# Optimization experiments

Hardware: AMD Instinct MI355X
Metric: run time of the kernel (lower is better)

## Reference

```python
import jax, jax.numpy as jnp
import numpy as np

N = 6144      # num_sample / nodes per graph
E = 196608    # edges per graph (avg degree 32)
F = 256       # input feature dim (same for all 4 graphs)
H = 256       # hidden_channels (== F so all SAGEConv layers are HxH)
D = 512       # fusion dim (hardcoded in module)
G = 4         # number of graphs
ATT = 128     # attention bottleneck (hardcoded)
WS = 0.05     # weight init scale


def setup_inputs() -> dict:
    key = jax.random.key(0)
    k = jax.random.split(key, 16)
    return {
        "xs": jax.random.normal(k[0], (G, N, F), jnp.float32),
        "edge_index": jax.random.randint(k[1], (G, 2, E), 0, N),
        "x_content": jax.random.normal(k[2], (N, F), jnp.float32),
        # SAGEConv params: per graph, 3 layers, lin_l (with bias) on aggregated
        # neighbors, lin_r (no bias) on root. F == H so all layers stack.
        "sage_Wl": jax.random.normal(k[3], (G, 3, H, H), jnp.float32) * WS,
        "sage_bl": jnp.zeros((G, 3, H), jnp.float32),
        "sage_Wr": jax.random.normal(k[4], (G, 3, H, H), jnp.float32) * WS,
        # lin1..lin4 : F -> 512
        "lin_W": jax.random.normal(k[5], (G, D, F), jnp.float32) * WS,
        "lin_b": jnp.zeros((G, D), jnp.float32),
        # ResidualFusion attention MLP 512 -> 128 -> 1, softmax over graph axis
        "att_W1": jax.random.normal(k[6], (ATT, D), jnp.float32) * WS,
        "att_b1": jnp.zeros((ATT,), jnp.float32),
        "att_W2": jax.random.normal(k[7], (1, ATT), jnp.float32) * WS,
        "att_b2": jnp.zeros((1,), jnp.float32),
        "res_W": jax.random.normal(k[8], (D, D), jnp.float32) * WS,
        "res_b": jnp.zeros((D,), jnp.float32),
        "fusion_weight": jnp.array([0.7, 0.3], jnp.float32),
        # SelfExpression coefficients, init 1e-8 * ones as in the module
        "C_content": jnp.full((N, N), 1e-8, jnp.float32),
        "C_structure": jnp.full((N, N), 1e-8, jnp.float32),
    }


def _gnn(x, ei, Wl, bl, Wr):
    # One GraphSAGE stack: 3 SAGEConv(mean) layers, relu after each,
    # dropout is identity in eval mode.
    src, dst = ei[0], ei[1]
    deg = jax.ops.segment_sum(jnp.ones((E,), x.dtype), dst, num_segments=N)
    deg = jnp.maximum(deg, 1.0)[:, None]
    for i in range(3):
        m = jax.ops.segment_sum(x[src], dst, num_segments=N) / deg  # mean aggr
        x = jax.nn.relu(m @ Wl[i].T + bl[i] + x @ Wr[i].T)
    return x


def reference(xs, edge_index, x_content, sage_Wl, sage_bl, sage_Wr,
              lin_W, lin_b, att_W1, att_b1, att_W2, att_b2,
              res_W, res_b, fusion_weight, C_content, C_structure):
    # Four GraphSAGE stacks, vmapped over the graph axis.
    xg = jax.vmap(_gnn)(xs, edge_index, sage_Wl, sage_bl, sage_Wr)  # [G,N,F]
    # lin1..lin4 -> [G,N,D]
    feats = jnp.einsum('gnf,gdf->gnd', xg, lin_W) + lin_b[:, None, :]
    # ResidualFusion: attention over stacked features, softmax over graph axis
    h = jax.nn.relu(jnp.einsum('gnd,kd->gnk', feats, att_W1) + att_b1)
    logits = jnp.einsum('gnk,ok->gno', h, att_W2) + att_b2  # [G,N,1]
    w = jax.nn.softmax(logits, axis=0)
    weighted = jnp.sum(w * feats, axis=0)            # [N,D]
    residual = feats[0] @ res_W.T + res_b            # [N,D]
    structure_features = jax.nn.relu(weighted + residual)
    # Coefficient fusion with softmax-normalized scalar weights
    fw = jax.nn.softmax(fusion_weight)
    fusion_expression = fw[0] * C_content + fw[1] * C_structure  # [N,N]
    return (fusion_expression, x_content, structure_features, C_content, C_structure)
```

## Files before the change

### kernel.cpp

```cpp
#include <hip/hip_runtime.h>
#include <hip/hip_bf16.h>

constexpr int N_ = 6144;
constexpr int E_ = 196608;
constexpr int F_ = 256;
constexpr int D_ = 512;
constexpr int G_ = 4;
constexpr int A_ = 128;

typedef short bf16x8 __attribute__((ext_vector_type(8)));
typedef float f32x4 __attribute__((ext_vector_type(4)));
typedef float f4 __attribute__((ext_vector_type(4)));
typedef int i4 __attribute__((ext_vector_type(4)));
typedef __hip_bfloat16 hb;

__device__ inline float b2f(unsigned short u) {
    union { unsigned u32; float f; } x; x.u32 = ((unsigned)u) << 16; return x.f;
}
__device__ inline unsigned short f2bu(float f) {
    hb b = __float2bfloat16(f);
    return *reinterpret_cast<unsigned short*>(&b);
}

#define GLD_LDS16(gp, lp) \
    __builtin_amdgcn_global_load_lds((const __attribute__((address_space(1))) void*)(gp), \
                                     (__attribute__((address_space(3))) void*)(lp), 16, 0, 0)

struct SP {
    const f4* Cc; const f4* Cs; const float* fw;
    f4* o0; f4* o3; f4* o4;
    long ib; long ie; int nsb;
};

__device__ void stream_slice(const SP sp, int sb)
{
    float fa = sp.fw[0], fb = sp.fw[1];
    float mx = fmaxf(fa, fb);
    float ea = expf(fa - mx), eb = expf(fb - mx);
    float w0 = ea / (ea + eb), w1 = eb / (ea + eb);
    const long S = (long)sp.nsb * blockDim.x;
    long i = sp.ib + (long)sb * blockDim.x + threadIdx.x;
    for (; i + 3 * S < sp.ie; i += 4 * S) {
        f4 a0 = __builtin_nontemporal_load(sp.Cc + i);
        f4 b0 = __builtin_nontemporal_load(sp.Cs + i);
        f4 a1 = __builtin_nontemporal_load(sp.Cc + i + S);
        f4 b1 = __builtin_nontemporal_load(sp.Cs + i + S);
        f4 a2 = __builtin_nontemporal_load(sp.Cc + i + 2 * S);
        f4 b2 = __builtin_nontemporal_load(sp.Cs + i + 2 * S);
        f4 a3 = __builtin_nontemporal_load(sp.Cc + i + 3 * S);
        f4 b3 = __builtin_nontemporal_load(sp.Cs + i + 3 * S);
        __builtin_nontemporal_store(a0, sp.o3 + i);
        __builtin_nontemporal_store(b0, sp.o4 + i);
        __builtin_nontemporal_store(w0 * a0 + w1 * b0, sp.o0 + i);
        __builtin_nontemporal_store(a1, sp.o3 + i + S);
        __builtin_nontemporal_store(b1, sp.o4 + i + S);
        __builtin_nontemporal_store(w0 * a1 + w1 * b1, sp.o0 + i + S);
        __builtin_nontemporal_store(a2, sp.o3 + i + 2 * S);
        __builtin_nontemporal_store(b2, sp.o4 + i + 2 * S);
        __builtin_nontemporal_store(w0 * a2 + w1 * b2, sp.o0 + i + 2 * S);
        __builtin_nontemporal_store(a3, sp.o3 + i + 3 * S);
        __builtin_nontemporal_store(b3, sp.o4 + i + 3 * S);
        __builtin_nontemporal_store(w0 * a3 + w1 * b3, sp.o0 + i + 3 * S);
    }
    for (; i < sp.ie; i += S) {
        f4 a = __builtin_nontemporal_load(sp.Cc + i);
        f4 b = __builtin_nontemporal_load(sp.Cs + i);
        __builtin_nontemporal_store(a, sp.o3 + i);
        __builtin_nontemporal_store(b, sp.o4 + i);
        __builtin_nontemporal_store(w0 * a + w1 * b, sp.o0 + i);
    }
}

__global__ void k_tail(SP sp) { stream_slice(sp, blockIdx.x); }

__global__ void k_prep(const float* __restrict__ xc, f4* __restrict__ o1,
                       const float* __restrict__ xs, ushort4* __restrict__ xsb,
                       const float* __restrict__ Wl, ushort4* __restrict__ Wlb,
                       const float* __restrict__ Wr, ushort4* __restrict__ Wrb,
                       const float* __restrict__ lin, ushort4* __restrict__ linb,
                       const float* __restrict__ aw, ushort4* __restrict__ awb,
                       const float* __restrict__ rw, ushort4* __restrict__ rwb,
                       i4* __restrict__ cursz, int PB, SP sp)
{
    if ((int)blockIdx.x < sp.nsb) { stream_slice(sp, blockIdx.x); return; }
    const int cb = blockIdx.x - sp.nsb;
    const long nz = (long)G_ * N_ / 4;
    const long n0 = (long)N_ * F_ / 4;
    const long n1 = (long)G_ * N_ * F_ / 4;
    const long n2 = (long)G_ * 3 * F_ * F_ / 4;
    const long n4 = (long)G_ * D_ * F_ / 4;
    const long n5 = (long)A_ * D_ / 4;
    const long n6 = (long)D_ * D_ / 4;
    const long T = nz + n0 + n1 + 2 * n2 + n4 + n5 + n6;
    long stride = (long)PB * blockDim.x;
    for (long u = (long)cb * blockDim.x + threadIdx.x; u < T; u += stride) {
        long v = u;
        if (v < nz) { cursz[v] = i4{0, 0, 0, 0}; continue; }
        v -= nz;
        if (v < n0) {
            f4 x = __builtin_nontemporal_load((const f4*)xc + v);
            __builtin_nontemporal_store(x, o1 + v);
            continue;
        }
        v -= n0;
        const float* s; ushort4* d;
        if (v < n1) { s = xs; d = xsb; }
        else {
            v -= n1;
            if (v < n2) { s = Wl; d = Wlb; }
            else {
                v -= n2;
                if (v < n2) { s = Wr; d = Wrb; }
                else {
                    v -= n2;
                    if (v < n4) { s = lin; d = linb; }
                    else {
                        v -= n4;
                        if (v < n5) { s = aw; d = awb; }
                        else { v -= n5; s = rw; d = rwb; }
                    }
                }
            }
        }
        f4 x = *((const f4*)s + v);
        ushort4 o;
        o.x = f2bu(x[0]); o.y = f2bu(x[1]); o.z = f2bu(x[2]); o.w = f2bu(x[3]);
        d[v] = o;
    }
}

__global__ void k_count(const int* __restrict__ ei, int* __restrict__ cnt, SP sp)
{
    if ((int)blockIdx.x < sp.nsb) { stream_slice(sp, blockIdx.x); return; }
    long i = (long)(blockIdx.x - sp.nsb) * blockDim.x + threadIdx.x;
    int g = (int)(i / E_);
    int e = (int)(i % E_);
    int dst = ei[(long)g * 2 * E_ + E_ + e];
    atomicAdd(&cnt[g * N_ + dst], 1);
}

__global__ void k_scan(int* __restrict__ cnt_cursor, int* __restrict__ row_ptr,
                       float* __restrict__ deg, SP sp)
{
    if ((int)blockIdx.x < sp.nsb) { stream_slice(sp, blockIdx.x); return; }
    int g = blockIdx.x - sp.nsb;
    __shared__ int sdata[1024];
    __shared__ int s_off;
    if (threadIdx.x == 0) s_off = 0;
    __syncthreads();
    for (int base = 0; base < N_; base += 1024) {
        int idx = g * N_ + base + threadIdx.x;
        int v = cnt_cursor[idx];
        sdata[threadIdx.x] = v;
        __syncthreads();
        for (int d = 1; d < 1024; d <<= 1) {
            int t = (threadIdx.x >= d) ? sdata[threadIdx.x - d] : 0;
            __syncthreads();
            sdata[threadIdx.x] += t;
            __syncthreads();
        }
        int incl = sdata[threadIdx.x];
        int excl = incl - v;
        int rp = s_off + excl;
        row_ptr[g * (N_ + 1) + base + threadIdx.x] = rp;
        cnt_cursor[idx] = rp;
        deg[idx] = (float)(v > 1 ? v : 1);
        __syncthreads();
        if (threadIdx.x == 1023) s_off += incl;
        __syncthreads();
    }
    if (threadIdx.x == 0) row_ptr[g * (N_ + 1) + N_] = s_off;
}

__global__ void k_fill(const int* __restrict__ ei, int* __restrict__ cursor,
                       int* __restrict__ csr_src, SP sp)
{
    if ((int)blockIdx.x < sp.nsb) { stream_slice(sp, blockIdx.x); return; }
    long i = (long)(blockIdx.x - sp.nsb) * blockDim.x + threadIdx.x;
    int g = (int)(i / E_);
    int e = (int)(i % E_);
    int src = ei[(long)g * 2 * E_ + e];
    int dst = ei[(long)g * 2 * E_ + E_ + e];
    int pos = atomicAdd(&cursor[g * N_ + dst], 1);
    csr_src[(long)g * E_ + pos] = src;
}

__global__ __launch_bounds__(256) void k_aggregate(
    const hb* __restrict__ x, const int* __restrict__ csr_src,
    const int* __restrict__ row_ptr, const float* __restrict__ deg,
    hb* __restrict__ m, SP sp)
{
    if ((int)blockIdx.x < sp.nsb) { stream_slice(sp, blockIdx.x); return; }
    int b = blockIdx.x - sp.nsb;
    int g = (b & 7) >> 1;
    int idx = ((b >> 3) << 1) | (b & 1);
    int node = idx * 4 + (threadIdx.x >> 6);
    int lane = threadIdx.x & 63;
    int qq = lane >> 4;
    int l16 = (lane & 15) * 16;
    const hb* xg = x + (long)g * N_ * F_;
    const int* rp = row_ptr + g * (N_ + 1);
    const int* cs = csr_src + (long)g * E_;
    int s = __builtin_amdgcn_readfirstlane(rp[node]);
    int e = __builtin_amdgcn_readfirstlane(rp[node + 1]);
    float a[16] = {};
    #pragma unroll 2
    for (int j = s; j < e; j += 4) {
        if (j + qq < e) {
            int src = cs[j + qq];
            const bf16x8* p = (const bf16x8*)(xg + (long)src * F_ + l16);
            bf16x8 v0 = p[0], v1 = p[1];
            #pragma unroll
            for (int q = 0; q < 8; ++q) a[q]     += b2f((unsigned short)v0[q]);
            #pragma unroll
            for (int q = 0; q < 8; ++q) a[q + 8] += b2f((unsigned short)v1[q]);
        }
    }
    #pragma unroll
    for (int q = 0; q < 16; ++q) {
        a[q] += __shfl_xor(a[q], 16);
        a[q] += __shfl_xor(a[q], 32);
    }
    if (qq == 0) {
        float inv = 1.0f / deg[g * N_ + node];
        bf16x8 lo, hi;
        #pragma unroll
        for (int q = 0; q < 8; ++q) { lo[q] = (short)f2bu(a[q] * inv); hi[q] = (short)f2bu(a[q + 8] * inv); }
        *(bf16x8*)(m + ((long)g * N_ + node) * F_ + l16) = lo;
        *(bf16x8*)(m + ((long)g * N_ + node) * F_ + l16 + 8) = hi;
    }
}

template <bool DUAL, bool RELU, bool LOGITS, bool FUSEOUT, bool PIN>
__global__ __launch_bounds__(256) void k_mfma_nt(
    const hb* __restrict__ A1, const hb* __restrict__ B1,
    const hb* __restrict__ A2, const hb* __restrict__ B2,
    const float* __restrict__ bias, hb* __restrict__ C,
    int ncols, int nrows, int ng, int Nc, int K,
    long a_batch, long b_batch, long bias_batch, long c_batch,
    const float* __restrict__ W2, const float* __restrict__ b2,
    float* __restrict__ logits,
    const float* __restrict__ lgAll, const hb* __restrict__ fAll,
    float* __restrict__ o2,
    SP sp)
{
    if ((int)blockIdx.x < sp.nsb) { stream_slice(sp, blockIdx.x); return; }
    int b = blockIdx.x - sp.nsb;
    int g, col, row;
    if (PIN) {
        g = (b & 7) >> 1;
        int idx = ((b >> 3) << 1) | (b & 1);
        col = idx % ncols; row = idx / ncols;
    } else {
        col = b % ncols;
        int r2 = b / ncols;
        row = r2 % nrows; g = r2 / nrows;
    }
    const int row0 = row * 128;
    const int col0 = col * 128;

    const hb* A1p = A1 + (long)g * a_batch;
    const hb* B1p = B1 + (long)g * b_batch;
    const hb* A2p = nullptr;
    const hb* B2p = nullptr;
    if (DUAL) { A2p = A2 + (long)g * a_batch; B2p = B2 + (long)g * b_batch; }
    const float* biasp = bias + (long)g * bias_batch;
    hb* Cp = C + (long)g * c_batch;

    __shared__ hb As[128 * 64];
    __shared__ hb Bs[128 * 64];
    __shared__ float sLog[2][128];
    __shared__ float sW[128][4];

    const int tid = threadIdx.x;
    const int lane = tid & 63;
    const int wid = tid >> 6;
    const int wr = wid >> 1;
    const int wc = wid & 1;

    if (FUSEOUT) {
        if (tid < 128) {
            int rr = row0 + tid;
            float l0 = lgAll[rr], l1 = lgAll[N_ + rr], l2 = lgAll[2 * N_ + rr], l3 = lgAll[3 * N_ + rr];
            float mx = fmaxf(fmaxf(l0, l1), fmaxf(l2, l3));
            float e0 = expf(l0 - mx), e1 = expf(l1 - mx), e2 = expf(l2 - mx), e3 = expf(l3 - mx);
            float inv = 1.f / (e0 + e1 + e2 + e3);
            sW[tid][0] = e0 * inv; sW[tid][1] = e1 * inv;
            sW[tid][2] = e2 * inv; sW[tid][3] = e3 * inv;
        }
    }

    const int srow = tid >> 3;
    const int sk8  = (tid & 7) * 8;

    f32x4 acc[4][4] = {};

    const int fr  = lane & 15;
    const int fkq = (lane >> 4) * 8;

    const int npass = DUAL ? 2 : 1;
    for (int pass = 0; pass < npass; ++pass) {
        const hb* A = (DUAL && pass) ? A2p : A1p;
        const hb* B = (DUAL && pass) ? B2p : B1p;
        for (int k0 = 0; k0 < K; k0 += 64) {
            __syncthreads();
            #pragma unroll
            for (int c = 0; c < 4; ++c) {
                int r = c * 32 + srow;
                GLD_LDS16(A + (long)(row0 + r) * K + k0 + sk8, As + r * 64 + sk8);
                GLD_LDS16(B + (long)(col0 + r) * K + k0 + sk8, Bs + r * 64 + sk8);
            }
            __syncthreads();

            bf16x8 af[4][2], bfr[4][2];
            #pragma unroll
            for (int m = 0; m < 4; ++m)
                #pragma unroll
                for (int kk = 0; kk < 2; ++kk)
                    af[m][kk] = *(const bf16x8*)(As + (wr * 64 + m * 16 + fr) * 64 + kk * 32 + fkq);
            #pragma unroll
            for (int n = 0; n < 4; ++n)
                #pragma unroll
                for (int kk = 0; kk < 2; ++kk)
                    bfr[n][kk] = *(const bf16x8*)(Bs + (wc * 64 + n * 16 + fr) * 64 + kk * 32 + fkq);

            #pragma unroll
            for (int m = 0; m < 4; ++m)
                #pragma unroll
                for (int n = 0; n < 4; ++n)
                    #pragma unroll
                    for (int kk = 0; kk < 2; ++kk)
                        acc[m][n] = __builtin_amdgcn_mfma_f32_16x16x32_bf16(
                            af[m][kk], bfr[n][kk], acc[m][n], 0, 0, 0);
        }
    }

    const int r4 = (lane >> 4) * 4;
    const int cc = lane & 15;

    if (LOGITS) {
        float w2v[4], bv[4];
        #pragma unroll
        for (int n = 0; n < 4; ++n) {
            int c2 = wc * 64 + n * 16 + cc;
            w2v[n] = W2[c2];
            bv[n]  = biasp[c2];
        }
        #pragma unroll
        for (int m = 0; m < 4; ++m) {
            #pragma unroll
            for (int j = 0; j < 4; ++j) {
                float p = 0.f;
                #pragma unroll
                for (int n = 0; n < 4; ++n) {
                    float h = fmaxf(acc[m][n][j] + bv[n], 0.f);
                    p += h * w2v[n];
                }
                p += __shfl_xor(p, 1); p += __shfl_xor(p, 2);
                p += __shfl_xor(p, 4); p += __shfl_xor(p, 8);
                if (cc == 0) sLog[wc][wr * 64 + m * 16 + r4 + j] = p;
            }
        }
        __syncthreads();
        if (tid < 128)
            logits[(long)g * N_ + row0 + tid] = sLog[0][tid] + sLog[1][tid] + b2[0];
    } else if (FUSEOUT) {
        const unsigned short* fu = (const unsigned short*)fAll;
        #pragma unroll
        for (int m = 0; m < 4; ++m) {
            #pragma unroll
            for (int n = 0; n < 4; ++n) {
                int c2 = col0 + wc * 64 + n * 16 + cc;
                float bv = biasp[c2];
                #pragma unroll
                for (int j = 0; j < 4; ++j) {
                    int rl = wr * 64 + m * 16 + r4 + j;
                    int rr = row0 + rl;
                    float s = acc[m][n][j] + bv;
                    #pragma unroll
                    for (int gg = 0; gg < 4; ++gg)
                        s += sW[rl][gg] * b2f(fu[((long)gg * N_ + rr) * D_ + c2]);
                    __builtin_nontemporal_store(fmaxf(s, 0.f), o2 + (long)rr * D_ + c2);
                }
            }
        }
    } else {
        #pragma unroll
        for (int m = 0; m < 4; ++m) {
            #pragma unroll
            for (int n = 0; n < 4; ++n) {
                int c2 = col0 + wc * 64 + n * 16 + cc;
                float bv = biasp[c2];
                #pragma unroll
                for (int j = 0; j < 4; ++j) {
                    int rr = row0 + wr * 64 + m * 16 + r4 + j;
                    float v = acc[m][n][j] + bv;
                    if (RELU) v = fmaxf(v, 0.f);
                    Cp[(long)rr * Nc + c2] = __float2bfloat16(v);
                }
            }
        }
    }
}

extern "C" void kernel_launch(void* const* d_in, const int* in_sizes, int n_in,
                              void* d_out, int out_size, void* d_ws, size_t ws_size,
                              hipStream_t stream)
{
    const float* xs        = (const float*)d_in[0];
    const int*   ei        = (const int*)  d_in[1];
    const float* x_content = (const float*)d_in[2];
    const float* sage_Wl   = (const float*)d_in[3];
    const float* sage_bl   = (const float*)d_in[4];
    const float* sage_Wr   = (const float*)d_in[5];
    const float* lin_W     = (const float*)d_in[6];
    const float* lin_b     = (const float*)d_in[7];
    const float* att_W1    = (const float*)d_in[8];
    const float* att_b1    = (const float*)d_in[9];
    const float* att_W2    = (const float*)d_in[10];
    const float* att_b2    = (const float*)d_in[11];
    const float* res_W     = (const float*)d_in[12];
    const float* res_b     = (const float*)d_in[13];
    const float* fusion_w  = (const float*)d_in[14];
    const float* Cc        = (const float*)d_in[15];
    const float* Cs        = (const float*)d_in[16];

    float* out0 = (float*)d_out;
    float* out1 = out0 + (size_t)N_ * N_;
    float* out2 = out1 + (size_t)N_ * F_;
    float* out3 = out2 + (size_t)N_ * D_;
    float* out4 = out3 + (size_t)N_ * N_;

    char* w = (char*)d_ws;
    auto alloc = [&](size_t bytes) {
        char* p = w;
        w += (bytes + 255) & ~(size_t)255;
        return p;
    };
    hb* xsb   = (hb*)alloc((size_t)G_ * N_ * F_ * 2);
    hb* xA    = (hb*)alloc((size_t)G_ * N_ * F_ * 2);
    hb* xB    = (hb*)alloc((size_t)G_ * N_ * F_ * 2);
    hb* mb    = (hb*)alloc((size_t)G_ * N_ * F_ * 2);
    hb* feats = (hb*)alloc((size_t)G_ * N_ * D_ * 2);
    hb* Wlb   = (hb*)alloc((size_t)G_ * 3 * F_ * F_ * 2);
    hb* Wrb   = (hb*)alloc((size_t)G_ * 3 * F_ * F_ * 2);
    hb* linWb = (hb*)alloc((size_t)G_ * D_ * F_ * 2);
    hb* attWb = (hb*)alloc((size_t)A_ * D_ * 2);
    hb* resWb = (hb*)alloc((size_t)D_ * D_ * 2);
    float* logit = (float*)alloc((size_t)G_ * N_ * 4);
    float* deg   = (float*)alloc((size_t)G_ * N_ * 4);
    int*   rowp  = (int*)  alloc((size_t)G_ * (N_ + 1) * 4);
    int*   curs  = (int*)  alloc((size_t)G_ * N_ * 4);
    int*   csrc  = (int*)  alloc((size_t)G_ * E_ * 4);

    const long U = (long)N_ * N_ / 4;
    const int cum[14] = {0, 85, 115, 135, 175, 285, 360, 470, 545, 655, 730, 820, 870, 975};
    long B[14];
    for (int i = 0; i < 14; ++i) B[i] = U * cum[i] / 1000;
    const int PREPB   = 512;
    const int SB_PREP = 512;
    const int SB_FLAT = 256;
    const int SB_GEMM = 256;
    const int TAILB   = 1024;
    auto mkSP = [&](int i, int nsb) {
        SP sp;
        sp.Cc = (const f4*)Cc; sp.Cs = (const f4*)Cs; sp.fw = fusion_w;
        sp.o0 = (f4*)out0; sp.o3 = (f4*)out3; sp.o4 = (f4*)out4;
        sp.ib = B[i]; sp.ie = (i == 13) ? U : B[i + 1]; sp.nsb = nsb;
        return sp;
    };
    SP tail = mkSP(13, TAILB);

    k_prep<<<SB_PREP + PREPB, 256, 0, stream>>>(
        x_content, (f4*)out1, xs, (ushort4*)xsb,
        sage_Wl, (ushort4*)Wlb, sage_Wr, (ushort4*)Wrb,
        lin_W, (ushort4*)linWb, att_W1, (ushort4*)attWb, res_W, (ushort4*)resWb,
        (i4*)curs, PREPB, mkSP(0, SB_PREP));

    k_count<<<SB_FLAT + G_ * E_ / 256, 256, 0, stream>>>(ei, curs, mkSP(1, SB_FLAT));
    k_scan<<<SB_FLAT + G_, 1024, 0, stream>>>(curs, rowp, deg, mkSP(2, SB_FLAT));
    k_fill<<<SB_FLAT + G_ * E_ / 256, 256, 0, stream>>>(ei, curs, csrc, mkSP(3, SB_FLAT));

    const hb* xin = xsb;
    hb* xout = xA;
    for (int layer = 0; layer < 3; ++layer) {
        k_aggregate<<<SB_FLAT + G_ * N_ / 4, 256, 0, stream>>>(
            xin, csrc, rowp, deg, mb, mkSP(4 + 2 * layer, SB_FLAT));
        k_mfma_nt<true, true, false, false, true>
            <<<SB_GEMM + (F_ / 128) * (N_ / 128) * G_, 256, 0, stream>>>(
            mb, Wlb + (size_t)layer * F_ * F_,
            xin, Wrb + (size_t)layer * F_ * F_,
            sage_bl + (size_t)layer * F_, xout,
            F_ / 128, N_ / 128, G_, F_, F_,
            (long)N_ * F_, (long)3 * F_ * F_, (long)3 * F_, (long)N_ * F_,
            nullptr, nullptr, nullptr, nullptr, nullptr, nullptr,
            mkSP(5 + 2 * layer, SB_GEMM));
        xin = xout;
        xout = (layer == 0) ? xB : xA;
    }
    const hb* xg = xA;

    k_mfma_nt<false, false, false, false, true>
        <<<SB_GEMM + (D_ / 128) * (N_ / 128) * G_, 256, 0, stream>>>(
        xg, linWb, nullptr, nullptr, lin_b, feats,
        D_ / 128, N_ / 128, G_, D_, F_,
        (long)N_ * F_, (long)D_ * F_, (long)D_, (long)N_ * D_,
        nullptr, nullptr, nullptr, nullptr, nullptr, nullptr,
        mkSP(10, SB_GEMM));

    k_mfma_nt<false, true, true, false, true>
        <<<SB_GEMM + (A_ / 128) * (N_ / 128) * G_, 256, 0, stream>>>(
        feats, attWb, nullptr, nullptr, att_b1, nullptr,
        A_ / 128, N_ / 128, G_, A_, D_,
        (long)N_ * D_, 0L, 0L, 0L,
        att_W2, att_b2, logit, nullptr, nullptr, nullptr,
        mkSP(11, SB_GEMM));

    k_mfma_nt<false, false, false, true, false>
        <<<SB_GEMM + (D_ / 128) * (N_ / 128) * 1, 256, 0, stream>>>(
        feats, resWb, nullptr, nullptr, res_b, nullptr,
        D_ / 128, N_ / 128, 1, D_, D_,
        0L, 0L, 0L, 0L,
        nullptr, nullptr, nullptr, logit, feats, out2,
        mkSP(12, SB_GEMM));

    k_tail<<<TAILB, 256, 0, stream>>>(tail);
}
```

Measured before the change: 428.0 us.

## Use wave-shuffle scan in k_scan, unroll aggregation loop, rebalance stream slices

The per-graph prefix scan replaces a 1024-wide shared-memory Hillis-Steele scan, which needed about 20 barriers per chunk, with a wavefront shuffle scan plus a small 16-entry cross-wave scan. This cuts the number of barriers and the LDS traffic in k_scan. The neighbor-aggregation loop unroll goes from 2 to 4 to keep more gathers in flight, at some register cost. The cumulative split that assigns the large N×N output streaming work to each kernel is also retuned, moving more work into the tail kernel.

Result: no change. 422.9 us (-1.2%).

```diff
diff --git a/kernel.cpp b/kernel.cpp
--- a/kernel.cpp
+++ b/kernel.cpp
@@ -144,29 +144,41 @@
 {
     if ((int)blockIdx.x < sp.nsb) { stream_slice(sp, blockIdx.x); return; }
     int g = blockIdx.x - sp.nsb;
-    __shared__ int sdata[1024];
+    __shared__ int swsum[16];
     __shared__ int s_off;
+    const int lane = threadIdx.x & 63;
+    const int wid = threadIdx.x >> 6;
     if (threadIdx.x == 0) s_off = 0;
     __syncthreads();
     for (int base = 0; base < N_; base += 1024) {
         int idx = g * N_ + base + threadIdx.x;
         int v = cnt_cursor[idx];
-        sdata[threadIdx.x] = v;
+        int incl = v;
+        #pragma unroll
+        for (int d = 1; d < 64; d <<= 1) {
+            int t = __shfl_up(incl, d);
+            if (lane >= d) incl += t;
+        }
+        if (lane == 63) swsum[wid] = incl;
         __syncthreads();
-        for (int d = 1; d < 1024; d <<= 1) {
-            int t = (threadIdx.x >= d) ? sdata[threadIdx.x - d] : 0;
-            __syncthreads();
-            sdata[threadIdx.x] += t;
-            __syncthreads();
-        }
-        int incl = sdata[threadIdx.x];
-        int excl = incl - v;
-        int rp = s_off + excl;
+        if (wid == 0 && lane < 16) {
+            int sv = swsum[lane];
+            #pragma unroll
+            for (int d = 1; d < 16; d <<= 1) {
+                int t = __shfl_up(sv, d);
+                if (lane >= d) sv += t;
+            }
+            swsum[lane] = sv;
+        }
+        __syncthreads();
+        int bse = s_off;
+        int woff = wid ? swsum[wid - 1] : 0;
+        int rp = bse + woff + incl - v;
         row_ptr[g * (N_ + 1) + base + threadIdx.x] = rp;
         cnt_cursor[idx] = rp;
         deg[idx] = (float)(v > 1 ? v : 1);
         __syncthreads();
-        if (threadIdx.x == 1023) s_off += incl;
+        if (threadIdx.x == 0) s_off = bse + swsum[15];
         __syncthreads();
     }
     if (threadIdx.x == 0) row_ptr[g * (N_ + 1) + N_] = s_off;
@@ -204,7 +216,7 @@
     int s = __builtin_amdgcn_readfirstlane(rp[node]);
     int e = __builtin_amdgcn_readfirstlane(rp[node + 1]);
     float a[16] = {};
-    #pragma unroll 2
+    #pragma unroll 4
     for (int j = s; j < e; j += 4) {
         if (j + qq < e) {
             int src = cs[j + qq];
@@ -454,7 +466,7 @@
     int*   csrc  = (int*)  alloc((size_t)G_ * E_ * 4);
 
     const long U = (long)N_ * N_ / 4;
-    const int cum[14] = {0, 85, 115, 135, 175, 285, 360, 470, 545, 655, 730, 820, 870, 975};
+    const int cum[14] = {0, 85, 110, 130, 160, 255, 325, 420, 490, 585, 655, 745, 815, 950};
     long B[14];
     for (int i = 0; i < 14; ++i) B[i] = U * cum[i] / 1000;
     const int PREPB   = 512;
```
